# Kernel tuning notes

Measured on AMD Instinct MI355X. Metric: run time of the kernel, lower is better.

The kernel has to match this reference:

```python
import jax, jax.numpy as jnp
import numpy as np

B = 4096          # number of sessions
MEAN_LEN = 50     # mean items per session
N = B * MEAN_LEN  # total items (ragged lengths sum to this)
H = 256           # feat_input_dim == context_input_dim == hidden_dim


def setup_inputs() -> dict:
    key = jax.random.key(0)
    k1, k2, k3, k4, k5, k6, k7 = jax.random.split(key, 7)
    # ragged lengths in [20, 80] adjusted so they sum exactly to N
    rng = np.random.default_rng(0)
    lens = rng.integers(20, 81, size=B)
    lens = (lens * (N / lens.sum())).astype(np.int64)
    lens[-1] += N - lens.sum()
    s = 1.0 / np.sqrt(H)
    return {
        "feats": jax.random.normal(k1, (N, H), jnp.float32),
        "feat_context": jax.random.normal(k2, (N, H), jnp.float32),
        "batch_num_items": jnp.asarray(lens, jnp.int64),
        "Wu": jax.random.uniform(k3, (H, H), jnp.float32, -s, s),
        "bu": jax.random.uniform(k4, (H,), jnp.float32, -s, s),
        "Wv": jax.random.uniform(k5, (H, H), jnp.float32, -s, s),
        "We": jax.random.uniform(k6, (H,), jnp.float32, -s, s),
        "Wout": jax.random.uniform(k7, (H, H), jnp.float32, -s, s),
    }


def reference(feats, feat_context, batch_num_items, Wu, bu, Wv, We, Wout):
    n = feats.shape[0]
    b = batch_num_items.shape[0]
    # additive attention score per item
    feat_u = feats @ Wu.T + bu                     # [N, H]
    feat_v = feat_context @ Wv.T                   # [N, H]
    e = jax.nn.sigmoid(feat_u + feat_v) @ We       # [N]
    # segment ids from ragged lengths (static total length => jit-safe)
    seg = jnp.repeat(jnp.arange(b), batch_num_items, total_repeat_length=n)
    # segment softmax (numerically stable)
    m = jax.ops.segment_max(e, seg, num_segments=b)        # [B]
    ex = jnp.exp(e - m[seg])                               # [N]
    denom = jax.ops.segment_sum(ex, seg, num_segments=b)   # [B]
    alpha = ex / denom[seg]                                # [N]
    # weighted segment-sum pooling
    rst = jax.ops.segment_sum(feats * alpha[:, None], seg, num_segments=b)  # [B, H]
    return rst @ Wout.T
```

## Files before the change

kernel.cpp:

```cpp
#include <hip/hip_runtime.h>
#include <cstdint>
#include <cstddef>

#define H 256
#define LDA2 72
#define CHUNK 128

typedef __attribute__((ext_vector_type(8))) short  frag8;
typedef __attribute__((ext_vector_type(8))) unsigned short ushort8;
typedef __attribute__((ext_vector_type(4))) float  f32x4;

__device__ __forceinline__ unsigned short f32_to_bf16(float f) {
    uint32_t u = __float_as_uint(f);
    u = (u + 0x7FFFu + ((u >> 16) & 1u)) >> 16;
    return (unsigned short)u;
}

__global__ void prep(const float* __restrict__ Wu, const float* __restrict__ Wv,
                     const float* __restrict__ Wout,
                     unsigned short* __restrict__ Wopt, float* __restrict__ WoutT) {
    int bid = blockIdx.x, tid = threadIdx.x;
    if (bid < 64) {
        int idx  = bid * 256 + tid;
        int lane = idx & 63;
        int ksg  = (idx >> 6) & 15;
        int ct   = idx >> 10;
        int col  = ct * 16 + (lane & 15);
        int kg   = ksg * 32 + (lane >> 4) * 8;
        ushort8 pk;
        #pragma unroll
        for (int j = 0; j < 8; j++) {
            int k = kg + j;
            float v = (k < 256) ? Wu[col * 256 + k] : Wv[col * 256 + (k - 256)];
            pk[j] = f32_to_bf16(v);
        }
        *(ushort8*)&Wopt[(size_t)idx * 8] = pk;
    } else {
        int t2 = (bid - 64) * 256 + tid;
        int j = t2 & 255, k = t2 >> 8;
        WoutT[t2] = Wout[j * 256 + k];
    }
}

__global__ void seg_offsets(const int* __restrict__ lens, int B, int* __restrict__ off,
                            int2* __restrict__ chunks, int* __restrict__ chunk_cnt) {
    __shared__ int partL[256], partC[256];
    int tid = threadIdx.x;
    bool is64 = (B >= 3) && (lens[1] == 0) && (lens[3] == 0) && (lens[5] == 0);
    int per = (B + 255) / 256;
    int base = tid * per;
    int sL = 0, sC = 0;
    for (int i = 0; i < per; i++) {
        int idx = base + i;
        if (idx < B) {
            int l = is64 ? lens[2 * idx] : lens[idx];
            sL += l;
            sC += (l + CHUNK - 1) / CHUNK;
        }
    }
    partL[tid] = sL; partC[tid] = sC;
    __syncthreads();
    for (int d = 1; d < 256; d <<= 1) {
        int vL = partL[tid], vC = partC[tid];
        int aL = (tid >= d) ? partL[tid - d] : 0;
        int aC = (tid >= d) ? partC[tid - d] : 0;
        __syncthreads();
        partL[tid] = vL + aL; partC[tid] = vC + aC;
        __syncthreads();
    }
    int runL = partL[tid] - sL;
    int runC = partC[tid] - sC;
    for (int i = 0; i < per; i++) {
        int idx = base + i;
        if (idx < B) {
            int l = is64 ? lens[2 * idx] : lens[idx];
            off[idx] = runL;
            int n = (l + CHUNK - 1) / CHUNK;
            for (int c = 0; c < n; c++)
                chunks[runC + c] = make_int2(idx, runL + c * CHUNK);
            runC += n;
            runL += l;
        }
    }
    if (tid == 255) { off[B] = partL[255]; chunk_cnt[0] = partC[255]; }
}

__global__ __launch_bounds__(256) void fused_e(
        const float* __restrict__ feats, const float* __restrict__ ctx,
        const unsigned short* __restrict__ Wopt,
        const float* __restrict__ bu, const float* __restrict__ We,
        float* __restrict__ e_out) {
    __shared__ unsigned short a_lds[64 * LDA2];
    __shared__ float e_part[4 * 64];

    const int tid  = threadIdx.x;
    const int lane = tid & 63;
    const int w    = tid >> 6;
    const int l15  = lane & 15;
    const int q    = lane >> 4;
    const size_t m0 = (size_t)blockIdx.x * 64;
    const int srow = tid >> 2;
    const int q4   = tid & 3;

    f32x4 acc[4][4];
    #pragma unroll
    for (int i = 0; i < 4; i++)
        #pragma unroll
        for (int j = 0; j < 4; j++)
            acc[i][j] = (f32x4)(0.0f);

    f32x4 pre[4];
    {
        const float* p = feats + (m0 + srow) * H + q4 * 16;
        pre[0] = *(const f32x4*)p;       pre[1] = *(const f32x4*)(p + 4);
        pre[2] = *(const f32x4*)(p + 8); pre[3] = *(const f32x4*)(p + 12);
    }

    for (int kt = 0; kt < 8; ++kt) {
        ushort8 lo, hi;
        #pragma unroll
        for (int j = 0; j < 4; j++) {
            lo[j]     = f32_to_bf16(pre[0][j]);
            lo[j + 4] = f32_to_bf16(pre[1][j]);
            hi[j]     = f32_to_bf16(pre[2][j]);
            hi[j + 4] = f32_to_bf16(pre[3][j]);
        }
        __syncthreads();
        *(ushort8*)&a_lds[srow * LDA2 + q4 * 16]     = lo;
        *(ushort8*)&a_lds[srow * LDA2 + q4 * 16 + 8] = hi;
        __syncthreads();

        if (kt < 7) {
            int ktn = kt + 1;
            const float* src = (ktn < 4) ? feats : ctx;
            const float* p = src + (m0 + srow) * H + (ktn & 3) * 64 + q4 * 16;
            pre[0] = *(const f32x4*)p;       pre[1] = *(const f32x4*)(p + 4);
            pre[2] = *(const f32x4*)(p + 8); pre[3] = *(const f32x4*)(p + 12);
        }

        #pragma unroll
        for (int ks = 0; ks < 2; ++ks) {
            const int ksg = kt * 2 + ks;
            frag8 afr[4], bfr[4];
            #pragma unroll
            for (int ci = 0; ci < 4; ++ci)
                bfr[ci] = *(const frag8*)&Wopt[((((size_t)(w * 4 + ci) * 16) + ksg) * 64 + lane) * 8];
            #pragma unroll
            for (int rt = 0; rt < 4; ++rt)
                afr[rt] = *(const frag8*)&a_lds[(rt * 16 + l15) * LDA2 + ks * 32 + q * 8];
            #pragma unroll
            for (int rt = 0; rt < 4; ++rt)
                #pragma unroll
                for (int ci = 0; ci < 4; ++ci)
                    acc[rt][ci] = __builtin_amdgcn_mfma_f32_16x16x32_bf16(
                        afr[rt], bfr[ci], acc[rt][ci], 0, 0, 0);
        }
    }

    float buv[4], wev[4];
    #pragma unroll
    for (int ci = 0; ci < 4; ++ci) {
        int col = w * 64 + ci * 16 + l15;
        buv[ci] = bu[col];
        wev[ci] = We[col];
    }
    #pragma unroll
    for (int rt = 0; rt < 4; ++rt) {
        #pragma unroll
        for (int r = 0; r < 4; ++r) {
            float s = 0.0f;
            #pragma unroll
            for (int ci = 0; ci < 4; ++ci) {
                float h = acc[rt][ci][r] + buv[ci];
                s += wev[ci] / (1.0f + __expf(-h));
            }
            s += __shfl_xor(s, 1, 64);
            s += __shfl_xor(s, 2, 64);
            s += __shfl_xor(s, 4, 64);
            s += __shfl_xor(s, 8, 64);
            if (l15 == 0) e_part[w * 64 + rt * 16 + q * 4 + r] = s;
        }
    }
    __syncthreads();
    if (tid < 64)
        e_out[m0 + tid] = e_part[tid] + e_part[64 + tid] + e_part[128 + tid] + e_part[192 + tid];
}

__global__ __launch_bounds__(256) void seg_stats(
        const float* __restrict__ e, const int* __restrict__ off, int B,
        float* __restrict__ m_arr, float* __restrict__ inv_arr) {
    int seg = blockIdx.x * 4 + (threadIdx.x >> 6);
    int lane = threadIdx.x & 63;
    if (seg >= B) return;
    int start = off[seg];
    int len = off[seg + 1] - start;
    float m = -3.0e38f;
    for (int i = lane; i < len; i += 64) m = fmaxf(m, e[start + i]);
    #pragma unroll
    for (int o = 32; o > 0; o >>= 1) m = fmaxf(m, __shfl_xor(m, o, 64));
    float s = 0.0f;
    for (int i = lane; i < len; i += 64) s += expf(e[start + i] - m);
    #pragma unroll
    for (int o = 32; o > 0; o >>= 1) s += __shfl_xor(s, o, 64);
    if (lane == 0) {
        m_arr[seg] = m;
        inv_arr[seg] = (s > 0.0f) ? 1.0f / s : 0.0f;
    }
}

__global__ __launch_bounds__(256) void pool_chunks(
        const float* __restrict__ e, const float* __restrict__ feats,
        const int* __restrict__ off, const int2* __restrict__ chunks,
        const int* __restrict__ chunk_cnt,
        const float* __restrict__ m_arr, const float* __restrict__ inv_arr,
        float* __restrict__ rst) {
    __shared__ float redf[4 * 256];
    int idx = blockIdx.x;
    if (idx >= chunk_cnt[0]) return;
    int2 en = chunks[idx];
    int seg = en.x, cstart = en.y;
    int sstart = off[seg], send = off[seg + 1];
    int clen = send - cstart;
    if (clen > CHUNK) clen = CHUNK;
    float m = m_arr[seg], inv = inv_arr[seg];
    int tid = threadIdx.x, lane = tid & 63, g = tid >> 6;

    f32x4 acc = (f32x4)(0.0f);
    const f32x4* feats4 = (const f32x4*)feats;
    for (int i = g; i < clen; i += 4) {
        float a = expf(e[cstart + i] - m) * inv;
        acc += a * feats4[(size_t)(cstart + i) * 64 + lane];
    }
    *(f32x4*)&redf[g * 256 + lane * 4] = acc;
    __syncthreads();
    float v = redf[tid] + redf[256 + tid] + redf[512 + tid] + redf[768 + tid];
    if (send - sstart > CHUNK) atomicAdd(&rst[(size_t)seg * H + tid], v);
    else rst[(size_t)seg * H + tid] = v;
}

#define RB 8
__global__ __launch_bounds__(256) void out_gemm(
        const float* __restrict__ rst, const float* __restrict__ WoutT,
        float* __restrict__ out) {
    __shared__ float r[RB * 256];
    const int tid = threadIdx.x;
    const size_t b0 = (size_t)blockIdx.x * RB;
    for (int i = tid; i < RB * 256; i += 256) r[i] = rst[b0 * 256 + i];
    __syncthreads();
    float acc[RB];
    #pragma unroll
    for (int j = 0; j < RB; j++) acc[j] = 0.0f;
    for (int k = 0; k < 256; k += 4) {
        f32x4 rw[RB];
        #pragma unroll
        for (int j = 0; j < RB; j++) rw[j] = *(const f32x4*)&r[j * 256 + k];
        #pragma unroll
        for (int kk = 0; kk < 4; kk++) {
            float wv = WoutT[(size_t)(k + kk) * 256 + tid];
            #pragma unroll
            for (int j = 0; j < RB; j++) acc[j] += rw[j][kk] * wv;
        }
    }
    #pragma unroll
    for (int j = 0; j < RB; j++) out[(b0 + j) * 256 + tid] = acc[j];
}

extern "C" void kernel_launch(void* const* d_in, const int* in_sizes, int n_in,
                              void* d_out, int out_size, void* d_ws, size_t ws_size,
                              hipStream_t stream) {
    const float* feats = (const float*)d_in[0];
    const float* ctx   = (const float*)d_in[1];
    const int*   lens  = (const int*)d_in[2];
    const float* Wu    = (const float*)d_in[3];
    const float* bu    = (const float*)d_in[4];
    const float* Wv    = (const float*)d_in[5];
    const float* We    = (const float*)d_in[6];
    const float* Wout  = (const float*)d_in[7];
    float* out = (float*)d_out;

    const int N = in_sizes[0] / H;
    const int B = in_sizes[2];
    const int maxChunks = B + (N + CHUNK - 1) / CHUNK;

    char* w = (char*)d_ws;
    auto carve = [&](size_t bytes) {
        char* p = w;
        w += (bytes + 255) & ~(size_t)255;
        return p;
    };
    int*            off    = (int*)           carve((size_t)(B + 1) * sizeof(int));
    float*          e      = (float*)         carve((size_t)N * sizeof(float));
    float*          rst    = (float*)         carve((size_t)B * H * sizeof(float));
    unsigned short* Wopt   = (unsigned short*)carve((size_t)16 * 16 * 64 * 8 * sizeof(unsigned short));
    float*          WoutT  = (float*)         carve((size_t)H * H * sizeof(float));
    int2*           chunks = (int2*)          carve((size_t)maxChunks * sizeof(int2));
    int*            ccnt   = (int*)           carve(sizeof(int));
    float*          m_arr  = (float*)         carve((size_t)B * sizeof(float));
    float*          i_arr  = (float*)         carve((size_t)B * sizeof(float));

    hipMemsetAsync(rst, 0, (size_t)B * H * sizeof(float), stream);

    prep        <<<320,           256, 0, stream>>>(Wu, Wv, Wout, Wopt, WoutT);
    seg_offsets <<<1,             256, 0, stream>>>(lens, B, off, chunks, ccnt);
    fused_e     <<<N / 64,        256, 0, stream>>>(feats, ctx, Wopt, bu, We, e);
    seg_stats   <<<(B + 3) / 4,   256, 0, stream>>>(e, off, B, m_arr, i_arr);
    pool_chunks <<<maxChunks,     256, 0, stream>>>(e, feats, off, chunks, ccnt, m_arr, i_arr, rst);
    out_gemm    <<<B / RB,        256, 0, stream>>>(rst, WoutT, out);
}
```

Baseline: 561.7 us.

## Widen GEMM k-tile with swizzled LDS, precompute alpha, unroll pooling loop

The fused attention-score GEMM now stages 128-wide K tiles (4 iterations instead of 8) into an XOR-swizzled, unpadded LDS layout. It converts to bf16 with packed intrinsics and reorders the weight fragment layout so each k-step's fragments sit contiguously. The segment-stats kernel writes the normalized softmax weights back in place, so pooling no longer recomputes exp per item, and the pooling loop is unrolled by two with dual accumulators. The sigmoid uses a hardware reciprocal. The aim is fewer barriers, fewer LDS bank conflicts and less redundant transcendental work, at the cost of more registers per thread for prefetch and slightly lower-precision math.

```diff
diff --git a/kernel.cpp b/kernel.cpp
--- a/kernel.cpp
+++ b/kernel.cpp
@@ -1,19 +1,26 @@
 #include <hip/hip_runtime.h>
+#include <hip/hip_bf16.h>
 #include <cstdint>
 #include <cstddef>
 
 #define H 256
-#define LDA2 72
 #define CHUNK 128
 
-typedef __attribute__((ext_vector_type(8))) short  frag8;
+typedef __attribute__((ext_vector_type(8))) short    frag8;
+typedef __attribute__((ext_vector_type(4))) float    f32x4;
+typedef __attribute__((ext_vector_type(4))) uint32_t u32x4;
 typedef __attribute__((ext_vector_type(8))) unsigned short ushort8;
-typedef __attribute__((ext_vector_type(4))) float  f32x4;
 
 __device__ __forceinline__ unsigned short f32_to_bf16(float f) {
     uint32_t u = __float_as_uint(f);
     u = (u + 0x7FFFu + ((u >> 16) & 1u)) >> 16;
     return (unsigned short)u;
+}
+
+__device__ __forceinline__ uint32_t pk_bf16(float a, float b) {
+    union { __hip_bfloat162 h2; uint32_t u; } cv;
+    cv.h2 = __float22bfloat162_rn(make_float2(a, b));
+    return cv.u;
 }
 
 __global__ void prep(const float* __restrict__ Wu, const float* __restrict__ Wv,
@@ -23,8 +30,8 @@
     if (bid < 64) {
         int idx  = bid * 256 + tid;
         int lane = idx & 63;
-        int ksg  = (idx >> 6) & 15;
-        int ct   = idx >> 10;
+        int ct   = (idx >> 6) & 15;
+        int ksg  = idx >> 10;
         int col  = ct * 16 + (lane & 15);
         int kg   = ksg * 32 + (lane >> 4) * 8;
         ushort8 pk;
@@ -90,7 +97,7 @@
         const unsigned short* __restrict__ Wopt,
         const float* __restrict__ bu, const float* __restrict__ We,
         float* __restrict__ e_out) {
-    __shared__ unsigned short a_lds[64 * LDA2];
+    __shared__ unsigned short a_lds[64 * 128];
     __shared__ float e_part[4 * 64];
 
     const int tid  = threadIdx.x;
@@ -99,8 +106,9 @@
     const int l15  = lane & 15;
     const int q    = lane >> 4;
     const size_t m0 = (size_t)blockIdx.x * 64;
-    const int srow = tid >> 2;
-    const int q4   = tid & 3;
+    const int r0   = tid >> 3;
+    const int c8   = tid & 7;
+    const int swz  = r0 & 15;
 
     f32x4 acc[4][4];
     #pragma unroll
@@ -109,45 +117,56 @@
         for (int j = 0; j < 4; j++)
             acc[i][j] = (f32x4)(0.0f);
 
-    f32x4 pre[4];
+    f32x4 pre[8];
     {
-        const float* p = feats + (m0 + srow) * H + q4 * 16;
-        pre[0] = *(const f32x4*)p;       pre[1] = *(const f32x4*)(p + 4);
-        pre[2] = *(const f32x4*)(p + 8); pre[3] = *(const f32x4*)(p + 12);
-    }
-
-    for (int kt = 0; kt < 8; ++kt) {
-        ushort8 lo, hi;
-        #pragma unroll
-        for (int j = 0; j < 4; j++) {
-            lo[j]     = f32_to_bf16(pre[0][j]);
-            lo[j + 4] = f32_to_bf16(pre[1][j]);
-            hi[j]     = f32_to_bf16(pre[2][j]);
-            hi[j + 4] = f32_to_bf16(pre[3][j]);
-        }
+        const float* pA = feats + (m0 + r0) * H + c8 * 16;
+        const float* pB = feats + (m0 + r0 + 32) * H + c8 * 16;
+        pre[0] = *(const f32x4*)pA;       pre[1] = *(const f32x4*)(pA + 4);
+        pre[2] = *(const f32x4*)(pA + 8); pre[3] = *(const f32x4*)(pA + 12);
+        pre[4] = *(const f32x4*)pB;       pre[5] = *(const f32x4*)(pB + 4);
+        pre[6] = *(const f32x4*)(pB + 8); pre[7] = *(const f32x4*)(pB + 12);
+    }
+
+    #pragma unroll
+    for (int kt = 0; kt < 4; ++kt) {
+        u32x4 g0, g1, g2, g3;
+        g0[0] = pk_bf16(pre[0][0], pre[0][1]); g0[1] = pk_bf16(pre[0][2], pre[0][3]);
+        g0[2] = pk_bf16(pre[1][0], pre[1][1]); g0[3] = pk_bf16(pre[1][2], pre[1][3]);
+        g1[0] = pk_bf16(pre[2][0], pre[2][1]); g1[1] = pk_bf16(pre[2][2], pre[2][3]);
+        g1[2] = pk_bf16(pre[3][0], pre[3][1]); g1[3] = pk_bf16(pre[3][2], pre[3][3]);
+        g2[0] = pk_bf16(pre[4][0], pre[4][1]); g2[1] = pk_bf16(pre[4][2], pre[4][3]);
+        g2[2] = pk_bf16(pre[5][0], pre[5][1]); g2[3] = pk_bf16(pre[5][2], pre[5][3]);
+        g3[0] = pk_bf16(pre[6][0], pre[6][1]); g3[1] = pk_bf16(pre[6][2], pre[6][3]);
+        g3[2] = pk_bf16(pre[7][0], pre[7][1]); g3[3] = pk_bf16(pre[7][2], pre[7][3]);
+
         __syncthreads();
-        *(ushort8*)&a_lds[srow * LDA2 + q4 * 16]     = lo;
-        *(ushort8*)&a_lds[srow * LDA2 + q4 * 16 + 8] = hi;
+        *(u32x4*)&a_lds[ r0       * 128 + (((2 * c8    ) ^ swz) * 8)] = g0;
+        *(u32x4*)&a_lds[ r0       * 128 + (((2 * c8 + 1) ^ swz) * 8)] = g1;
+        *(u32x4*)&a_lds[(r0 + 32) * 128 + (((2 * c8    ) ^ swz) * 8)] = g2;
+        *(u32x4*)&a_lds[(r0 + 32) * 128 + (((2 * c8 + 1) ^ swz) * 8)] = g3;
         __syncthreads();
 
-        if (kt < 7) {
-            int ktn = kt + 1;
-            const float* src = (ktn < 4) ? feats : ctx;
-            const float* p = src + (m0 + srow) * H + (ktn & 3) * 64 + q4 * 16;
-            pre[0] = *(const f32x4*)p;       pre[1] = *(const f32x4*)(p + 4);
-            pre[2] = *(const f32x4*)(p + 8); pre[3] = *(const f32x4*)(p + 12);
-        }
-
-        #pragma unroll
-        for (int ks = 0; ks < 2; ++ks) {
-            const int ksg = kt * 2 + ks;
+        if (kt < 3) {
+            const float* src = (kt + 1 < 2) ? feats : ctx;
+            const int kb = ((kt + 1) & 1) * 128;
+            const float* pA = src + (m0 + r0) * H + kb + c8 * 16;
+            const float* pB = src + (m0 + r0 + 32) * H + kb + c8 * 16;
+            pre[0] = *(const f32x4*)pA;       pre[1] = *(const f32x4*)(pA + 4);
+            pre[2] = *(const f32x4*)(pA + 8); pre[3] = *(const f32x4*)(pA + 12);
+            pre[4] = *(const f32x4*)pB;       pre[5] = *(const f32x4*)(pB + 4);
+            pre[6] = *(const f32x4*)(pB + 8); pre[7] = *(const f32x4*)(pB + 12);
+        }
+
+        #pragma unroll
+        for (int ks = 0; ks < 4; ++ks) {
+            const int ksg = kt * 4 + ks;
             frag8 afr[4], bfr[4];
             #pragma unroll
             for (int ci = 0; ci < 4; ++ci)
-                bfr[ci] = *(const frag8*)&Wopt[((((size_t)(w * 4 + ci) * 16) + ksg) * 64 + lane) * 8];
+                bfr[ci] = *(const frag8*)&Wopt[(((size_t)ksg * 16 + w * 4 + ci) * 64 + lane) * 8];
             #pragma unroll
             for (int rt = 0; rt < 4; ++rt)
-                afr[rt] = *(const frag8*)&a_lds[(rt * 16 + l15) * LDA2 + ks * 32 + q * 8];
+                afr[rt] = *(const frag8*)&a_lds[(rt * 16 + l15) * 128 + (((ks * 4 + q) ^ l15) * 8)];
             #pragma unroll
             for (int rt = 0; rt < 4; ++rt)
                 #pragma unroll
@@ -172,7 +191,7 @@
             #pragma unroll
             for (int ci = 0; ci < 4; ++ci) {
                 float h = acc[rt][ci][r] + buv[ci];
-                s += wev[ci] / (1.0f + __expf(-h));
+                s += wev[ci] * __builtin_amdgcn_rcpf(1.0f + __expf(-h));
             }
             s += __shfl_xor(s, 1, 64);
             s += __shfl_xor(s, 2, 64);
@@ -187,8 +206,7 @@
 }
 
 __global__ __launch_bounds__(256) void seg_stats(
-        const float* __restrict__ e, const int* __restrict__ off, int B,
-        float* __restrict__ m_arr, float* __restrict__ inv_arr) {
+        float* __restrict__ e, const int* __restrict__ off, int B) {
     int seg = blockIdx.x * 4 + (threadIdx.x >> 6);
     int lane = threadIdx.x & 63;
     if (seg >= B) return;
@@ -199,21 +217,17 @@
     #pragma unroll
     for (int o = 32; o > 0; o >>= 1) m = fmaxf(m, __shfl_xor(m, o, 64));
     float s = 0.0f;
-    for (int i = lane; i < len; i += 64) s += expf(e[start + i] - m);
+    for (int i = lane; i < len; i += 64) s += __expf(e[start + i] - m);
     #pragma unroll
     for (int o = 32; o > 0; o >>= 1) s += __shfl_xor(s, o, 64);
-    if (lane == 0) {
-        m_arr[seg] = m;
-        inv_arr[seg] = (s > 0.0f) ? 1.0f / s : 0.0f;
-    }
+    float inv = (s > 0.0f) ? 1.0f / s : 0.0f;
+    for (int i = lane; i < len; i += 64) e[start + i] = __expf(e[start + i] - m) * inv;
 }
 
 __global__ __launch_bounds__(256) void pool_chunks(
-        const float* __restrict__ e, const float* __restrict__ feats,
+        const float* __restrict__ alpha, const float* __restrict__ feats,
         const int* __restrict__ off, const int2* __restrict__ chunks,
-        const int* __restrict__ chunk_cnt,
-        const float* __restrict__ m_arr, const float* __restrict__ inv_arr,
-        float* __restrict__ rst) {
+        const int* __restrict__ chunk_cnt, float* __restrict__ rst) {
     __shared__ float redf[4 * 256];
     int idx = blockIdx.x;
     if (idx >= chunk_cnt[0]) return;
@@ -222,16 +236,19 @@
     int sstart = off[seg], send = off[seg + 1];
     int clen = send - cstart;
     if (clen > CHUNK) clen = CHUNK;
-    float m = m_arr[seg], inv = inv_arr[seg];
     int tid = threadIdx.x, lane = tid & 63, g = tid >> 6;
 
-    f32x4 acc = (f32x4)(0.0f);
-    const f32x4* feats4 = (const f32x4*)feats;
-    for (int i = g; i < clen; i += 4) {
-        float a = expf(e[cstart + i] - m) * inv;
-        acc += a * feats4[(size_t)(cstart + i) * 64 + lane];
-    }
-    *(f32x4*)&redf[g * 256 + lane * 4] = acc;
+    const f32x4* F = (const f32x4*)feats + (size_t)cstart * 64 + lane;
+    const float* A = alpha + cstart;
+    f32x4 acc0 = (f32x4)(0.0f), acc1 = (f32x4)(0.0f);
+    int i = g;
+    for (; i + 4 < clen; i += 8) {
+        acc0 += A[i]     * F[(size_t)i * 64];
+        acc1 += A[i + 4] * F[(size_t)(i + 4) * 64];
+    }
+    if (i < clen) acc0 += A[i] * F[(size_t)i * 64];
+    acc0 += acc1;
+    *(f32x4*)&redf[g * 256 + lane * 4] = acc0;
     __syncthreads();
     float v = redf[tid] + redf[256 + tid] + redf[512 + tid] + redf[768 + tid];
     if (send - sstart > CHUNK) atomicAdd(&rst[(size_t)seg * H + tid], v);
@@ -295,15 +312,13 @@
     float*          WoutT  = (float*)         carve((size_t)H * H * sizeof(float));
     int2*           chunks = (int2*)          carve((size_t)maxChunks * sizeof(int2));
     int*            ccnt   = (int*)           carve(sizeof(int));
-    float*          m_arr  = (float*)         carve((size_t)B * sizeof(float));
-    float*          i_arr  = (float*)         carve((size_t)B * sizeof(float));
 
     hipMemsetAsync(rst, 0, (size_t)B * H * sizeof(float), stream);
 
-    prep        <<<320,           256, 0, stream>>>(Wu, Wv, Wout, Wopt, WoutT);
-    seg_offsets <<<1,             256, 0, stream>>>(lens, B, off, chunks, ccnt);
-    fused_e     <<<N / 64,        256, 0, stream>>>(feats, ctx, Wopt, bu, We, e);
-    seg_stats   <<<(B + 3) / 4,   256, 0, stream>>>(e, off, B, m_arr, i_arr);
-    pool_chunks <<<maxChunks,     256, 0, stream>>>(e, feats, off, chunks, ccnt, m_arr, i_arr, rst);
-    out_gemm    <<<B / RB,        256, 0, stream>>>(rst, WoutT, out);
-}
+    prep        <<<320,         256, 0, stream>>>(Wu, Wv, Wout, Wopt, WoutT);
+    seg_offsets <<<1,           256, 0, stream>>>(lens, B, off, chunks, ccnt);
+    fused_e     <<<N / 64,      256, 0, stream>>>(feats, ctx, Wopt, bu, We, e);
+    seg_stats   <<<(B + 3) / 4, 256, 0, stream>>>(e, off, B);
+    pool_chunks <<<maxChunks,   256, 0, stream>>>(e, feats, off, chunks, ccnt, rst);
+    out_gemm    <<<B / RB,      256, 0, stream>>>(rst, WoutT, out);
+}
```

Result: faster. 537.3 us (-4.3%).
